# Kernel optimization log

Measured on AMD Instinct MI355X. Metric: run time of the kernel, lower is better.

## Reference

```python
import jax, jax.numpy as jnp
import numpy as np

N_HEAD = 8
N_FEAT = 512
D_HEAD = N_FEAT // N_HEAD


def setup_inputs() -> dict:
    key = jax.random.key(0)
    ks = jax.random.split(key, 11)
    B, T, L = 4, 2048, 16
    s = 1.0 / np.sqrt(D_HEAD)
    so = 1.0 / np.sqrt(N_FEAT)
    return {
        "q": jax.random.normal(ks[0], (B, T, 1, N_FEAT), jnp.float32),
        "k": jax.random.normal(ks[1], (B, T, L, N_FEAT), jnp.float32),
        "v": jax.random.normal(ks[2], (B, T, L, N_FEAT), jnp.float32),
        "Wq": jax.random.uniform(ks[3], (D_HEAD, D_HEAD), jnp.float32, -s, s),
        "bq": jax.random.uniform(ks[4], (D_HEAD,), jnp.float32, -s, s),
        "Wk": jax.random.uniform(ks[5], (D_HEAD, D_HEAD), jnp.float32, -s, s),
        "bk": jax.random.uniform(ks[6], (D_HEAD,), jnp.float32, -s, s),
        "Wv": jax.random.uniform(ks[7], (D_HEAD, D_HEAD), jnp.float32, -s, s),
        "bv": jax.random.uniform(ks[8], (D_HEAD,), jnp.float32, -s, s),
        "Wo": jax.random.uniform(ks[9], (N_FEAT, N_FEAT), jnp.float32, -so, so),
        "bo": jax.random.uniform(ks[10], (N_FEAT,), jnp.float32, -so, so),
    }


def reference(q, k, v, Wq, bq, Wk, bk, Wv, bv, Wo, bo):
    B, T, L, F = k.shape
    H, D = N_HEAD, D_HEAD
    # split heads: q [B,T,H,D] (query axis of length 1 squeezed), k/v [B,T,L,H,D]
    qh = q.reshape(B, T, H, D)
    kh = k.reshape(B, T, L, H, D)
    vh = v.reshape(B, T, L, H, D)
    # per-head linear projections (shared across heads), Linear: x @ W^T + b
    qh = jnp.einsum("bthd,ed->bthe", qh, Wq) + bq
    kh = jnp.einsum("btlhd,ed->btlhe", kh, Wk) + bk
    vh = jnp.einsum("btlhd,ed->btlhe", vh, Wv) + bv
    # attention scores over the local window L (query length 1 per timestep)
    attw = jnp.einsum("bthd,btlhd->bthl", qh, kh) / jnp.sqrt(jnp.asarray(D, qh.dtype))
    attn = jax.nn.softmax(attw, axis=-1)  # dropout is identity in eval mode
    ct = jnp.einsum("bthl,btlhd->bthd", attn, vh)
    ct = ct.reshape(B, T, F)
    return ct @ Wo.T + bo
```

## Files before the change

kernel.cpp:

```cpp
#include <hip/hip_runtime.h>


#define NFEAT 512
#define NHEAD 8
#define DHEAD 64
#define LWIN  16
#define WPOS  8
#define NBT   32

typedef __attribute__((ext_vector_type(8))) short bf16x8;
typedef __attribute__((ext_vector_type(4))) float f32x4;

__device__ __forceinline__ unsigned short f2bf(float f) {
    unsigned int u = __float_as_uint(f);
    unsigned int r = (u + 0x7fffu + ((u >> 16) & 1u)) >> 16;
    return (unsigned short)r;
}

__device__ __forceinline__ void gload16(const float* src, float* dst) {
    __builtin_amdgcn_global_load_lds((const __attribute__((address_space(1))) float*)src,
                                     (__attribute__((address_space(3))) float*)dst,
                                     16, 0, 0);
}
__device__ __forceinline__ void gload4(const float* src, float* dst) {
    __builtin_amdgcn_global_load_lds((const __attribute__((address_space(1))) float*)src,
                                     (__attribute__((address_space(3))) float*)dst,
                                     4, 0, 0);
}

__global__ void precompute_small(const float* __restrict__ Wq, const float* __restrict__ bq,
                                 const float* __restrict__ Wk,
                                 const float* __restrict__ Wo, const float* __restrict__ bo,
                                 const float* __restrict__ bv,
                                 float* __restrict__ A, float* __restrict__ g,
                                 float* __restrict__ b2) {
    int idx = blockIdx.x * 256 + threadIdx.x;
    if (idx < 4096) {
        int d = idx >> 6, dp = idx & 63;
        float s = 0.f;
        #pragma unroll 8
        for (int e = 0; e < 64; ++e) s = fmaf(Wq[e * 64 + d], Wk[e * 64 + dp], s);
        A[idx] = s;
    } else if (idx < 4160) {
        int dp = idx - 4096;
        float s = 0.f;
        #pragma unroll 8
        for (int e = 0; e < 64; ++e) s = fmaf(Wk[e * 64 + dp], bq[e], s);
        g[dp] = s;
    } else if (idx < 4672) {
        int j = idx - 4160;
        float s = bo[j];
        #pragma unroll 8
        for (int i = 0; i < 512; ++i) s = fmaf(Wo[j * 512 + i], bv[i & 63], s);
        b2[j] = s;
    }
}

__global__ void precompute_wo2(const float* __restrict__ Wo, const float* __restrict__ Wv,
                               unsigned short* __restrict__ Wo2B) {
    int idx = blockIdx.x * 256 + threadIdx.x;
    int i = idx & 511, j = idx >> 9;
    int h = i >> 6, e = i & 63;
    float s = 0.f;
    #pragma unroll 8
    for (int d = 0; d < 64; ++d)
        s = fmaf(Wo[j * 512 + h * 64 + d], Wv[d * 64 + e], s);
    Wo2B[(size_t)j * 512 + i] = f2bf(s);
}

__global__ __launch_bounds__(512, 4)
void w_prepass(const float* __restrict__ q, const float* __restrict__ A,
               const float* __restrict__ g, float* __restrict__ Wm) {
    __shared__ float As[4096];
    __shared__ float qs[WPOS][NFEAT];
    const int tid = threadIdx.x;
    const int bt0 = blockIdx.x * WPOS;

    #pragma unroll
    for (int i = 0; i < 8; ++i) As[i * 512 + tid] = A[i * 512 + tid];
    #pragma unroll
    for (int r = 0; r < WPOS; ++r) qs[r][tid] = q[(size_t)(bt0 + r) * NFEAT + tid];
    __syncthreads();

    const int e  = tid & 63;
    const int hb = (tid >> 6) << 6;
    float acc[WPOS];
    const float ge = g[e];
    #pragma unroll
    for (int r = 0; r < WPOS; ++r) acc[r] = ge;

    #pragma unroll 4
    for (int dq = 0; dq < 16; ++dq) {
        const float a0 = As[(4 * dq + 0) * 64 + e];
        const float a1 = As[(4 * dq + 1) * 64 + e];
        const float a2 = As[(4 * dq + 2) * 64 + e];
        const float a3 = As[(4 * dq + 3) * 64 + e];
        #pragma unroll
        for (int r = 0; r < WPOS; ++r) {
            const float4 qv = *reinterpret_cast<const float4*>(&qs[r][hb + 4 * dq]);
            acc[r] = fmaf(qv.x, a0, acc[r]);
            acc[r] = fmaf(qv.y, a1, acc[r]);
            acc[r] = fmaf(qv.z, a2, acc[r]);
            acc[r] = fmaf(qv.w, a3, acc[r]);
        }
    }
    #pragma unroll
    for (int r = 0; r < WPOS; ++r)
        Wm[(size_t)(bt0 + r) * NFEAT + tid] = acc[r] * 0.125f;
}

__global__ __launch_bounds__(512, 1)
void attn_stream(const float* __restrict__ Wm, const float* __restrict__ k,
                 const float* __restrict__ v, unsigned short* __restrict__ vbarG) {
    __shared__ __align__(16) float kbuf[2][LWIN][NFEAT];
    __shared__ __align__(16) float vbuf[2][LWIN][NFEAT];
    __shared__ __align__(16) float wmbuf[2][NFEAT];

    const int tid  = threadIdx.x;
    const int w    = tid >> 6;
    const int lane = tid & 63;
    const int lq   = lane >> 2;
    const int d4   = lane & 3;
    const int bt0  = blockIdx.x * NBT;

    #define ISSUE_TILE(buf, bti)                                                  \
    {                                                                             \
        const float* kb_ = k + (size_t)(bti) * (LWIN * NFEAT);                    \
        const float* vb_ = v + (size_t)(bti) * (LWIN * NFEAT);                    \
        _Pragma("unroll")                                                         \
        for (int rr = 0; rr < 2; ++rr) {                                          \
            const int r_    = 2 * w + rr;                                         \
            const int kofs_ = ((lane * 16) ^ ((r_ & 7) << 4)) >> 2;               \
            gload16(kb_ + r_ * NFEAT +       kofs_,     &kbuf[buf][r_][0]);       \
            gload16(kb_ + r_ * NFEAT + 256 + kofs_,     &kbuf[buf][r_][256]);     \
            gload16(vb_ + r_ * NFEAT +       lane * 4,  &vbuf[buf][r_][0]);       \
            gload16(vb_ + r_ * NFEAT + 256 + lane * 4,  &vbuf[buf][r_][256]);     \
        }                                                                         \
        gload4(Wm + (size_t)(bti) * NFEAT + w * 64 + lane, &wmbuf[buf][w * 64]);  \
    }

    ISSUE_TILE(0, bt0 + 0);
    ISSUE_TILE(1, bt0 + 1);

    const int half  = (w >> 2) & 1;
    const int hwoff = (w & 3) * 256 + d4 * 64;
    const int swz   = (lq & 7) << 4;

    for (int i = 0; i < NBT; ++i) {
        const int cur = i & 1;
        const int bt  = bt0 + i;

        if (i + 1 < NBT) {
            asm volatile("s_waitcnt vmcnt(9)" ::: "memory");
        } else {
            asm volatile("s_waitcnt vmcnt(1)" ::: "memory");
        }
        __builtin_amdgcn_sched_barrier(0);
        __builtin_amdgcn_s_barrier();
        __builtin_amdgcn_sched_barrier(0);

        const float* wmp = &wmbuf[cur][w * 64 + d4 * 16];
        const float4 wm0 = *(const float4*)(wmp + 0);
        const float4 wm1 = *(const float4*)(wmp + 4);
        const float4 wm2 = *(const float4*)(wmp + 8);
        const float4 wm3 = *(const float4*)(wmp + 12);

        const char* rowb = (const char*)&kbuf[cur][lq][0] + half * 1024;
        const float4 k0 = *(const float4*)(rowb + ((hwoff +  0) ^ swz));
        const float4 k1 = *(const float4*)(rowb + ((hwoff + 16) ^ swz));
        const float4 k2 = *(const float4*)(rowb + ((hwoff + 32) ^ swz));
        const float4 k3 = *(const float4*)(rowb + ((hwoff + 48) ^ swz));
        float s0 = wm0.x * k0.x, s1 = wm1.x * k1.x, s2 = wm2.x * k2.x, s3 = wm3.x * k3.x;
        s0 = fmaf(wm0.y, k0.y, s0); s1 = fmaf(wm1.y, k1.y, s1);
        s2 = fmaf(wm2.y, k2.y, s2); s3 = fmaf(wm3.y, k3.y, s3);
        s0 = fmaf(wm0.z, k0.z, s0); s1 = fmaf(wm1.z, k1.z, s1);
        s2 = fmaf(wm2.z, k2.z, s2); s3 = fmaf(wm3.z, k3.z, s3);
        s0 = fmaf(wm0.w, k0.w, s0); s1 = fmaf(wm1.w, k1.w, s1);
        s2 = fmaf(wm2.w, k2.w, s2); s3 = fmaf(wm3.w, k3.w, s3);
        float s = (s0 + s1) + (s2 + s3);
        s += __shfl_xor(s, 1, 64);
        s += __shfl_xor(s, 2, 64);
        const float e = __expf(s);

        float den = 0.f, acc = 0.f;
        #pragma unroll
        for (int l = 0; l < LWIN; ++l) {
            const float el = __shfl(e, 4 * l, 64);
            den += el;
            acc = fmaf(el, vbuf[cur][l][w * 64 + lane], acc);
        }
        vbarG[(size_t)bt * NFEAT + tid] = f2bf(acc * (1.0f / den));

        __builtin_amdgcn_sched_barrier(0);
        __builtin_amdgcn_s_barrier();
        __builtin_amdgcn_sched_barrier(0);

        if (i + 2 < NBT) {
            ISSUE_TILE(cur, bt + 2);
        }
        __builtin_amdgcn_sched_barrier(0);
    }
    #undef ISSUE_TILE
}

__global__ __launch_bounds__(512, 4)
void out_gemm(const unsigned short* __restrict__ vbarBF,
              const unsigned short* __restrict__ Wo2B,
              const float* __restrict__ b2, float* __restrict__ out) {
    const int tid  = threadIdx.x;
    const int w    = tid >> 6;
    const int lane = tid & 63;
    const int mt   = blockIdx.x;
    const int n0   = w * 64;
    const int r    = lane & 15;
    const int kg   = lane >> 4;

    const short* Ab  = (const short*)vbarBF + ((size_t)(mt * 16 + r)) * 512 + kg * 8;
    const short* Bb0 = (const short*)Wo2B + ((size_t)(n0 +  0 + r)) * 512 + kg * 8;
    const short* Bb1 = (const short*)Wo2B + ((size_t)(n0 + 16 + r)) * 512 + kg * 8;
    const short* Bb2 = (const short*)Wo2B + ((size_t)(n0 + 32 + r)) * 512 + kg * 8;
    const short* Bb3 = (const short*)Wo2B + ((size_t)(n0 + 48 + r)) * 512 + kg * 8;

    f32x4 acc0 = {0.f, 0.f, 0.f, 0.f}, acc1 = acc0, acc2 = acc0, acc3 = acc0;

    #pragma unroll 4
    for (int kk = 0; kk < 16; ++kk) {
        const bf16x8 a   = *reinterpret_cast<const bf16x8*>(Ab  + kk * 32);
        const bf16x8 b0  = *reinterpret_cast<const bf16x8*>(Bb0 + kk * 32);
        const bf16x8 b1  = *reinterpret_cast<const bf16x8*>(Bb1 + kk * 32);
        const bf16x8 b2v = *reinterpret_cast<const bf16x8*>(Bb2 + kk * 32);
        const bf16x8 b3  = *reinterpret_cast<const bf16x8*>(Bb3 + kk * 32);
        acc0 = __builtin_amdgcn_mfma_f32_16x16x32_bf16(a, b0,  acc0, 0, 0, 0);
        acc1 = __builtin_amdgcn_mfma_f32_16x16x32_bf16(a, b1,  acc1, 0, 0, 0);
        acc2 = __builtin_amdgcn_mfma_f32_16x16x32_bf16(a, b2v, acc2, 0, 0, 0);
        acc3 = __builtin_amdgcn_mfma_f32_16x16x32_bf16(a, b3,  acc3, 0, 0, 0);
    }

    const float bb0 = b2[n0 + 0 + r],  bb1 = b2[n0 + 16 + r];
    const float bb2 = b2[n0 + 32 + r], bb3 = b2[n0 + 48 + r];
    #pragma unroll
    for (int j = 0; j < 4; ++j) {
        const size_t row = (size_t)(mt * 16 + kg * 4 + j) * 512;
        out[row + n0 +  0 + r] = acc0[j] + bb0;
        out[row + n0 + 16 + r] = acc1[j] + bb1;
        out[row + n0 + 32 + r] = acc2[j] + bb2;
        out[row + n0 + 48 + r] = acc3[j] + bb3;
    }
}

extern "C" void kernel_launch(void* const* d_in, const int* in_sizes, int n_in,
                              void* d_out, int out_size, void* d_ws, size_t ws_size,
                              hipStream_t stream) {
    const float* q  = (const float*)d_in[0];
    const float* k  = (const float*)d_in[1];
    const float* v  = (const float*)d_in[2];
    const float* Wq = (const float*)d_in[3];
    const float* bq = (const float*)d_in[4];
    const float* Wk = (const float*)d_in[5];
    const float* Wv = (const float*)d_in[7];
    const float* bv = (const float*)d_in[8];
    const float* Wo = (const float*)d_in[9];
    const float* bo = (const float*)d_in[10];
    float* out = (float*)d_out;

    float* ws = (float*)d_ws;
    float*          A      = ws;
    float*          g      = ws + 4096;
    float*          b2     = ws + 4160;
    unsigned short* Wo2B   = (unsigned short*)(ws + 4672);
    float*          Wm     = ws + 4672 + 131072;
    unsigned short* vbarG  = (unsigned short*)(ws + 4672 + 131072 + 4194304);

    const int BT = in_sizes[0] / NFEAT;

    hipLaunchKernelGGL(precompute_small, dim3(19), dim3(256), 0, stream,
                       Wq, bq, Wk, Wo, bo, bv, A, g, b2);
    hipLaunchKernelGGL(precompute_wo2, dim3(1024), dim3(256), 0, stream,
                       Wo, Wv, Wo2B);
    hipLaunchKernelGGL(w_prepass, dim3(BT / WPOS), dim3(512), 0, stream,
                       q, A, g, Wm);
    hipLaunchKernelGGL(attn_stream, dim3(BT / NBT), dim3(512), 0, stream,
                       Wm, k, v, vbarG);
    hipLaunchKernelGGL(out_gemm, dim3(BT / 16), dim3(512), 0, stream,
                       vbarG, Wo2B, b2, out);
}
```

Before: 209.8 us.

## Fuse query projection and output GEMM into single streaming attention kernel

Merges the separate Wm prepass, attention streaming, and output GEMM kernels into one monolithic kernel. Each block computes the projected query per timestep from registers holding A, stages bf16 context rows in shared memory, and every 16 timesteps runs the MFMA output projection directly. This removes two kernel launches and the global round-trips for Wm and vbar. The cost is 64 extra registers per thread for A, more shared memory, and GEMM work serialized inside the streaming loop, where it can stall the k/v prefetch pipeline.

Result: faster. 179.0 us (-14.6%).

```diff
diff --git a/kernel.cpp b/kernel.cpp
--- a/kernel.cpp
+++ b/kernel.cpp
@@ -5,8 +5,8 @@
 #define NHEAD 8
 #define DHEAD 64
 #define LWIN  16
-#define WPOS  8
 #define NBT   32
+#define VPITCH 520
 
 typedef __attribute__((ext_vector_type(8))) short bf16x8;
 typedef __attribute__((ext_vector_type(4))) float f32x4;
@@ -68,53 +68,16 @@
     Wo2B[(size_t)j * 512 + i] = f2bf(s);
 }
 
-__global__ __launch_bounds__(512, 4)
-void w_prepass(const float* __restrict__ q, const float* __restrict__ A,
-               const float* __restrict__ g, float* __restrict__ Wm) {
-    __shared__ float As[4096];
-    __shared__ float qs[WPOS][NFEAT];
-    const int tid = threadIdx.x;
-    const int bt0 = blockIdx.x * WPOS;
-
-    #pragma unroll
-    for (int i = 0; i < 8; ++i) As[i * 512 + tid] = A[i * 512 + tid];
-    #pragma unroll
-    for (int r = 0; r < WPOS; ++r) qs[r][tid] = q[(size_t)(bt0 + r) * NFEAT + tid];
-    __syncthreads();
-
-    const int e  = tid & 63;
-    const int hb = (tid >> 6) << 6;
-    float acc[WPOS];
-    const float ge = g[e];
-    #pragma unroll
-    for (int r = 0; r < WPOS; ++r) acc[r] = ge;
-
-    #pragma unroll 4
-    for (int dq = 0; dq < 16; ++dq) {
-        const float a0 = As[(4 * dq + 0) * 64 + e];
-        const float a1 = As[(4 * dq + 1) * 64 + e];
-        const float a2 = As[(4 * dq + 2) * 64 + e];
-        const float a3 = As[(4 * dq + 3) * 64 + e];
-        #pragma unroll
-        for (int r = 0; r < WPOS; ++r) {
-            const float4 qv = *reinterpret_cast<const float4*>(&qs[r][hb + 4 * dq]);
-            acc[r] = fmaf(qv.x, a0, acc[r]);
-            acc[r] = fmaf(qv.y, a1, acc[r]);
-            acc[r] = fmaf(qv.z, a2, acc[r]);
-            acc[r] = fmaf(qv.w, a3, acc[r]);
-        }
-    }
-    #pragma unroll
-    for (int r = 0; r < WPOS; ++r)
-        Wm[(size_t)(bt0 + r) * NFEAT + tid] = acc[r] * 0.125f;
-}
-
 __global__ __launch_bounds__(512, 1)
-void attn_stream(const float* __restrict__ Wm, const float* __restrict__ k,
-                 const float* __restrict__ v, unsigned short* __restrict__ vbarG) {
+void attn_mono(const float* __restrict__ q, const float* __restrict__ k,
+               const float* __restrict__ v, const float* __restrict__ A,
+               const float* __restrict__ g, const unsigned short* __restrict__ Wo2B,
+               const float* __restrict__ b2, float* __restrict__ out) {
     __shared__ __align__(16) float kbuf[2][LWIN][NFEAT];
     __shared__ __align__(16) float vbuf[2][LWIN][NFEAT];
-    __shared__ __align__(16) float wmbuf[2][NFEAT];
+    __shared__ __align__(16) float qbuf[2][NFEAT];
+    __shared__ __align__(16) float wmbuf[NFEAT];
+    __shared__ __align__(16) unsigned short vbarS[16 * VPITCH];
 
     const int tid  = threadIdx.x;
     const int w    = tid >> 6;
@@ -122,6 +85,11 @@
     const int lq   = lane >> 2;
     const int d4   = lane & 3;
     const int bt0  = blockIdx.x * NBT;
+
+    float Areg[64];
+    #pragma unroll
+    for (int d = 0; d < 64; ++d) Areg[d] = A[d * 64 + lane];
+    const float greg = g[lane];
 
     #define ISSUE_TILE(buf, bti)                                                  \
     {                                                                             \
@@ -136,7 +104,7 @@
             gload16(vb_ + r_ * NFEAT +       lane * 4,  &vbuf[buf][r_][0]);       \
             gload16(vb_ + r_ * NFEAT + 256 + lane * 4,  &vbuf[buf][r_][256]);     \
         }                                                                         \
-        gload4(Wm + (size_t)(bti) * NFEAT + w * 64 + lane, &wmbuf[buf][w * 64]);  \
+        gload4(q + (size_t)(bti) * NFEAT + w * 64 + lane, &qbuf[buf][w * 64]);    \
     }
 
     ISSUE_TILE(0, bt0 + 0);
@@ -153,13 +121,28 @@
         if (i + 1 < NBT) {
             asm volatile("s_waitcnt vmcnt(9)" ::: "memory");
         } else {
-            asm volatile("s_waitcnt vmcnt(1)" ::: "memory");
+            asm volatile("s_waitcnt vmcnt(0)" ::: "memory");
         }
         __builtin_amdgcn_sched_barrier(0);
         __builtin_amdgcn_s_barrier();
         __builtin_amdgcn_sched_barrier(0);
 
-        const float* wmp = &wmbuf[cur][w * 64 + d4 * 16];
+        {
+            const float* qrow = &qbuf[cur][w * 64];
+            float c0 = 0.f, c1 = 0.f, c2 = 0.f, c3 = 0.f;
+            #pragma unroll
+            for (int d = 0; d < 64; d += 4) {
+                c0 = fmaf(qrow[d + 0], Areg[d + 0], c0);
+                c1 = fmaf(qrow[d + 1], Areg[d + 1], c1);
+                c2 = fmaf(qrow[d + 2], Areg[d + 2], c2);
+                c3 = fmaf(qrow[d + 3], Areg[d + 3], c3);
+            }
+            wmbuf[w * 64 + lane] = (greg + (c0 + c1) + (c2 + c3)) * 0.125f;
+        }
+        asm volatile("s_waitcnt lgkmcnt(0)" ::: "memory");
+        __builtin_amdgcn_sched_barrier(0);
+
+        const float* wmp = &wmbuf[w * 64 + d4 * 16];
         const float4 wm0 = *(const float4*)(wmp + 0);
         const float4 wm1 = *(const float4*)(wmp + 4);
         const float4 wm2 = *(const float4*)(wmp + 8);
@@ -182,15 +165,16 @@
         s += __shfl_xor(s, 2, 64);
         const float e = __expf(s);
 
-        float den = 0.f, acc = 0.f;
+        float den = 0.f, accv = 0.f;
         #pragma unroll
         for (int l = 0; l < LWIN; ++l) {
             const float el = __shfl(e, 4 * l, 64);
             den += el;
-            acc = fmaf(el, vbuf[cur][l][w * 64 + lane], acc);
-        }
-        vbarG[(size_t)bt * NFEAT + tid] = f2bf(acc * (1.0f / den));
-
+            accv = fmaf(el, vbuf[cur][l][w * 64 + lane], accv);
+        }
+        vbarS[(i & 15) * VPITCH + w * 64 + lane] = f2bf(accv * (1.0f / den));
+
+        asm volatile("s_waitcnt lgkmcnt(0)" ::: "memory");
         __builtin_amdgcn_sched_barrier(0);
         __builtin_amdgcn_s_barrier();
         __builtin_amdgcn_sched_barrier(0);
@@ -199,53 +183,46 @@
             ISSUE_TILE(cur, bt + 2);
         }
         __builtin_amdgcn_sched_barrier(0);
+
+        if ((i & 15) == 15) {
+            const int m0   = bt - 15;
+            const int n0   = w * 64;
+            const int r    = lane & 15;
+            const int kg   = lane >> 4;
+
+            const unsigned short* As0 = vbarS + r * VPITCH + kg * 8;
+            const short* Bb0 = (const short*)Wo2B + ((size_t)(n0 +  0 + r)) * 512 + kg * 8;
+            const short* Bb1 = (const short*)Wo2B + ((size_t)(n0 + 16 + r)) * 512 + kg * 8;
+            const short* Bb2 = (const short*)Wo2B + ((size_t)(n0 + 32 + r)) * 512 + kg * 8;
+            const short* Bb3 = (const short*)Wo2B + ((size_t)(n0 + 48 + r)) * 512 + kg * 8;
+
+            f32x4 acc0 = {0.f, 0.f, 0.f, 0.f}, acc1 = acc0, acc2 = acc0, acc3 = acc0;
+            #pragma unroll 4
+            for (int kk = 0; kk < 16; ++kk) {
+                const bf16x8 a   = *reinterpret_cast<const bf16x8*>(As0 + kk * 32);
+                const bf16x8 b0  = *reinterpret_cast<const bf16x8*>(Bb0 + kk * 32);
+                const bf16x8 b1  = *reinterpret_cast<const bf16x8*>(Bb1 + kk * 32);
+                const bf16x8 b2v = *reinterpret_cast<const bf16x8*>(Bb2 + kk * 32);
+                const bf16x8 b3  = *reinterpret_cast<const bf16x8*>(Bb3 + kk * 32);
+                acc0 = __builtin_amdgcn_mfma_f32_16x16x32_bf16(a, b0,  acc0, 0, 0, 0);
+                acc1 = __builtin_amdgcn_mfma_f32_16x16x32_bf16(a, b1,  acc1, 0, 0, 0);
+                acc2 = __builtin_amdgcn_mfma_f32_16x16x32_bf16(a, b2v, acc2, 0, 0, 0);
+                acc3 = __builtin_amdgcn_mfma_f32_16x16x32_bf16(a, b3,  acc3, 0, 0, 0);
+            }
+
+            const float bb0 = b2[n0 + 0 + r],  bb1 = b2[n0 + 16 + r];
+            const float bb2 = b2[n0 + 32 + r], bb3 = b2[n0 + 48 + r];
+            #pragma unroll
+            for (int j = 0; j < 4; ++j) {
+                const size_t row = (size_t)(m0 + kg * 4 + j) * 512;
+                out[row + n0 +  0 + r] = acc0[j] + bb0;
+                out[row + n0 + 16 + r] = acc1[j] + bb1;
+                out[row + n0 + 32 + r] = acc2[j] + bb2;
+                out[row + n0 + 48 + r] = acc3[j] + bb3;
+            }
+        }
     }
     #undef ISSUE_TILE
-}
-
-__global__ __launch_bounds__(512, 4)
-void out_gemm(const unsigned short* __restrict__ vbarBF,
-              const unsigned short* __restrict__ Wo2B,
-              const float* __restrict__ b2, float* __restrict__ out) {
-    const int tid  = threadIdx.x;
-    const int w    = tid >> 6;
-    const int lane = tid & 63;
-    const int mt   = blockIdx.x;
-    const int n0   = w * 64;
-    const int r    = lane & 15;
-    const int kg   = lane >> 4;
-
-    const short* Ab  = (const short*)vbarBF + ((size_t)(mt * 16 + r)) * 512 + kg * 8;
-    const short* Bb0 = (const short*)Wo2B + ((size_t)(n0 +  0 + r)) * 512 + kg * 8;
-    const short* Bb1 = (const short*)Wo2B + ((size_t)(n0 + 16 + r)) * 512 + kg * 8;
-    const short* Bb2 = (const short*)Wo2B + ((size_t)(n0 + 32 + r)) * 512 + kg * 8;
-    const short* Bb3 = (const short*)Wo2B + ((size_t)(n0 + 48 + r)) * 512 + kg * 8;
-
-    f32x4 acc0 = {0.f, 0.f, 0.f, 0.f}, acc1 = acc0, acc2 = acc0, acc3 = acc0;
-
-    #pragma unroll 4
-    for (int kk = 0; kk < 16; ++kk) {
-        const bf16x8 a   = *reinterpret_cast<const bf16x8*>(Ab  + kk * 32);
-        const bf16x8 b0  = *reinterpret_cast<const bf16x8*>(Bb0 + kk * 32);
-        const bf16x8 b1  = *reinterpret_cast<const bf16x8*>(Bb1 + kk * 32);
-        const bf16x8 b2v = *reinterpret_cast<const bf16x8*>(Bb2 + kk * 32);
-        const bf16x8 b3  = *reinterpret_cast<const bf16x8*>(Bb3 + kk * 32);
-        acc0 = __builtin_amdgcn_mfma_f32_16x16x32_bf16(a, b0,  acc0, 0, 0, 0);
-        acc1 = __builtin_amdgcn_mfma_f32_16x16x32_bf16(a, b1,  acc1, 0, 0, 0);
-        acc2 = __builtin_amdgcn_mfma_f32_16x16x32_bf16(a, b2v, acc2, 0, 0, 0);
-        acc3 = __builtin_amdgcn_mfma_f32_16x16x32_bf16(a, b3,  acc3, 0, 0, 0);
-    }
-
-    const float bb0 = b2[n0 + 0 + r],  bb1 = b2[n0 + 16 + r];
-    const float bb2 = b2[n0 + 32 + r], bb3 = b2[n0 + 48 + r];
-    #pragma unroll
-    for (int j = 0; j < 4; ++j) {
-        const size_t row = (size_t)(mt * 16 + kg * 4 + j) * 512;
-        out[row + n0 +  0 + r] = acc0[j] + bb0;
-        out[row + n0 + 16 + r] = acc1[j] + bb1;
-        out[row + n0 + 32 + r] = acc2[j] + bb2;
-        out[row + n0 + 48 + r] = acc3[j] + bb3;
-    }
 }
 
 extern "C" void kernel_launch(void* const* d_in, const int* in_sizes, int n_in,
@@ -264,12 +241,10 @@
     float* out = (float*)d_out;
 
     float* ws = (float*)d_ws;
-    float*          A      = ws;
-    float*          g      = ws + 4096;
-    float*          b2     = ws + 4160;
-    unsigned short* Wo2B   = (unsigned short*)(ws + 4672);
-    float*          Wm     = ws + 4672 + 131072;
-    unsigned short* vbarG  = (unsigned short*)(ws + 4672 + 131072 + 4194304);
+    float*          A    = ws;
+    float*          g    = ws + 4096;
+    float*          b2   = ws + 4160;
+    unsigned short* Wo2B = (unsigned short*)(ws + 4672);
 
     const int BT = in_sizes[0] / NFEAT;
 
@@ -277,10 +252,6 @@
                        Wq, bq, Wk, Wo, bo, bv, A, g, b2);
     hipLaunchKernelGGL(precompute_wo2, dim3(1024), dim3(256), 0, stream,
                        Wo, Wv, Wo2B);
-    hipLaunchKernelGGL(w_prepass, dim3(BT / WPOS), dim3(512), 0, stream,
-                       q, A, g, Wm);
-    hipLaunchKernelGGL(attn_stream, dim3(BT / NBT), dim3(512), 0, stream,
-                       Wm, k, v, vbarG);
-    hipLaunchKernelGGL(out_gemm, dim3(BT / 16), dim3(512), 0, stream,
-                       vbarG, Wo2B, b2, out);
-}
+    hipLaunchKernelGGL(attn_mono, dim3(BT / NBT), dim3(512), 0, stream,
+                       q, k, v, A, g, Wo2B, b2, out);
+}
```
